# Kernel tuning notes

Hardware: AMD Instinct MI355X
Metric: run time of the kernel (lower is better)

## Reference

```python
import jax, jax.numpy as jnp
import numpy as np

B, S, F, HS = 64, 512, 512, 1024


def _xavier(key, shape):
    fan_in, fan_out = shape
    limit = np.sqrt(6.0 / (fan_in + fan_out))
    return jax.random.uniform(key, shape, jnp.float32, -limit, limit)


def setup_inputs() -> dict:
    key = jax.random.key(0)
    k1, k2, k3 = jax.random.split(key, 3)
    x = jax.random.normal(k1, (B, S, F), jnp.float32)
    weight_ih = _xavier(k2, (F, 3 * HS))
    weight_hh = _xavier(k3, (HS, 3 * HS))
    # bias: zeros except the r-gate slice [HS:2HS] initialized to ones (per init_weights)
    bias = jnp.zeros((3 * HS,), jnp.float32).at[HS:2 * HS].set(1.0)
    return {"x": x, "weight_ih": weight_ih, "weight_hh": weight_hh, "bias": bias}


def reference(x, weight_ih, weight_hh, bias):
    hs = weight_hh.shape[0]
    bsz = x.shape[0]
    # Precompute input-side gates for all timesteps; bias folds in additively
    # (for eta gate: gx_e + r*tanh(gh_e) + b_e  ==  (gx_e + b_e) + r*tanh(gh_e)).
    gx = jnp.einsum('bsf,fg->bsg', x, weight_ih) + bias  # [B,S,3H]

    def step(h, gx_t):
        gh = h @ weight_hh  # [B,3H]
        z = jax.nn.sigmoid(gx_t[:, :hs] + gh[:, :hs])
        r = jax.nn.sigmoid(gx_t[:, hs:2 * hs] + gh[:, hs:2 * hs])
        eta = jnp.tanh(gx_t[:, 2 * hs:] + r * jnp.tanh(gh[:, 2 * hs:]))
        h_new = z * h + (1.0 - z) * eta
        return h_new, h_new

    h0 = jnp.zeros((bsz, hs), x.dtype)
    h_last, hseq = jax.lax.scan(step, h0, jnp.swapaxes(gx, 0, 1))  # hseq: [S,B,H]
    hidden_seq = jnp.swapaxes(hseq, 0, 1)  # [B,S,H]
    return hidden_seq, h_last
```

## Files before the change

kernel.cpp:

```cpp
#include <hip/hip_runtime.h>
#include <math.h>


#define B_   64
#define S_   512
#define F_   512
#define H_   1024
#define KTOT 1536
#define NG   4096
#define NWG  256
#define NTHR 512
#define RS   1544
#define CPS  324
#define SMEM_BYTES (2 * 16 * RS * 2 + 32 * CPS * 4)

typedef short short8 __attribute__((ext_vector_type(8)));
typedef float floatx4 __attribute__((ext_vector_type(4)));

__device__ __forceinline__ float bf2f(unsigned short u) {
    union { unsigned int i; float f; } v; v.i = ((unsigned int)u) << 16; return v.f;
}
__device__ __forceinline__ unsigned short f2bf(float f) {
    union { float f; unsigned int i; } v; v.f = f;
    unsigned int x = v.i;
    x += 0x7fffu + ((x >> 16) & 1u);
    return (unsigned short)(x >> 16);
}
__device__ __forceinline__ void split2(float v, unsigned short& hi, unsigned short& lo) {
    hi = f2bf(v);
    lo = f2bf(v - bf2f(hi));
}
__device__ __forceinline__ float tanh_fast(float a) {
    float e = __expf(-2.f * fabsf(a));
    float t = (1.f - e) / (1.f + e);
    return copysignf(t, a);
}

__global__ void pack_w(const float* __restrict__ Wih,
                       const float* __restrict__ Whh,
                       unsigned short* __restrict__ Whi,
                       unsigned short* __restrict__ Wlo) {
    int idx = blockIdx.x * 256 + threadIdx.x;
    int p = idx / KTOT;
    int k = idx - p * KTOT;
    int j = p >> 2, g = p & 3;
    float v = 0.f;
    if (g == 0)      v = (k < F_) ? Wih[k * 3072 + j]        : Whh[(k - F_) * 3072 + j];
    else if (g == 1) v = (k < F_) ? Wih[k * 3072 + 1024 + j] : Whh[(k - F_) * 3072 + 1024 + j];
    else if (g == 2) { if (k <  F_) v = Wih[k * 3072 + 2048 + j]; }
    else             { if (k >= F_) v = Whh[(k - F_) * 3072 + 2048 + j]; }
    unsigned short hi, lo; split2(v, hi, lo);
    Whi[idx] = hi; Wlo[idx] = lo;
}

__global__ void pack_x(const float* __restrict__ x,
                       unsigned short* __restrict__ xhi,
                       unsigned short* __restrict__ xlo) {
    int idx = blockIdx.x * 256 + threadIdx.x;
    unsigned short hi, lo; split2(x[idx], hi, lo);
    xhi[idx] = hi; xlo[idx] = lo;
}

__device__ __forceinline__ void ks_step_x(floatx4* acc,
    const unsigned short* __restrict__ Ahi, const unsigned short* __restrict__ Alo,
    size_t aofs, const unsigned short* Bh_, const unsigned short* Bl_, int bofs)
{
    short8 bh = *(const short8*)&Bh_[bofs];
    short8 bl = *(const short8*)&Bl_[bofs];
    #pragma unroll
    for (int mt = 0; mt < 4; ++mt) {
        size_t o = aofs + (size_t)mt * ((size_t)16 * S_ * F_);
        short8 ah = *(const short8*)&Ahi[o];
        short8 al = *(const short8*)&Alo[o];
        acc[mt] = __builtin_amdgcn_mfma_f32_16x16x32_bf16(ah, bh, acc[mt], 0, 0, 0);
        acc[mt] = __builtin_amdgcn_mfma_f32_16x16x32_bf16(ah, bl, acc[mt], 0, 0, 0);
        acc[mt] = __builtin_amdgcn_mfma_f32_16x16x32_bf16(al, bh, acc[mt], 0, 0, 0);
    }
}

#define LOADH(A, OFS) \
    asm volatile( \
        "global_load_dwordx4 %0, %[q0], off offset:" OFS " sc0 sc1\n\t" \
        "global_load_dwordx4 %1, %[q1], off offset:" OFS " sc0 sc1\n\t" \
        "global_load_dwordx4 %2, %[q2], off offset:" OFS " sc0 sc1\n\t" \
        "global_load_dwordx4 %3, %[q3], off offset:" OFS " sc0 sc1\n\t" \
        "global_load_dwordx4 %4, %[q4], off offset:" OFS " sc0 sc1\n\t" \
        "global_load_dwordx4 %5, %[q5], off offset:" OFS " sc0 sc1\n\t" \
        "global_load_dwordx4 %6, %[q6], off offset:" OFS " sc0 sc1\n\t" \
        "global_load_dwordx4 %7, %[q7], off offset:" OFS " sc0 sc1" \
        : "=&v"(A[0]), "=&v"(A[1]), "=&v"(A[2]), "=&v"(A[3]), \
          "=&v"(A[4]), "=&v"(A[5]), "=&v"(A[6]), "=&v"(A[7]) \
        : [q0]"v"(ph0), [q1]"v"(pl0), [q2]"v"(ph1), [q3]"v"(pl1), \
          [q4]"v"(ph2), [q5]"v"(pl2), [q6]"v"(ph3), [q7]"v"(pl3) \
        : "memory")

#define WAITVM(N) do { \
        asm volatile("s_waitcnt vmcnt(" #N ")" ::: "memory"); \
        __builtin_amdgcn_sched_barrier(0); \
    } while (0)

#define MFMAS(A, BH, BL) \
    acc[0] = __builtin_amdgcn_mfma_f32_16x16x32_bf16(A[0], BH, acc[0], 0, 0, 0); \
    acc[0] = __builtin_amdgcn_mfma_f32_16x16x32_bf16(A[0], BL, acc[0], 0, 0, 0); \
    acc[0] = __builtin_amdgcn_mfma_f32_16x16x32_bf16(A[1], BH, acc[0], 0, 0, 0); \
    acc[1] = __builtin_amdgcn_mfma_f32_16x16x32_bf16(A[2], BH, acc[1], 0, 0, 0); \
    acc[1] = __builtin_amdgcn_mfma_f32_16x16x32_bf16(A[2], BL, acc[1], 0, 0, 0); \
    acc[1] = __builtin_amdgcn_mfma_f32_16x16x32_bf16(A[3], BH, acc[1], 0, 0, 0); \
    acc[2] = __builtin_amdgcn_mfma_f32_16x16x32_bf16(A[4], BH, acc[2], 0, 0, 0); \
    acc[2] = __builtin_amdgcn_mfma_f32_16x16x32_bf16(A[4], BL, acc[2], 0, 0, 0); \
    acc[2] = __builtin_amdgcn_mfma_f32_16x16x32_bf16(A[5], BH, acc[2], 0, 0, 0); \
    acc[3] = __builtin_amdgcn_mfma_f32_16x16x32_bf16(A[6], BH, acc[3], 0, 0, 0); \
    acc[3] = __builtin_amdgcn_mfma_f32_16x16x32_bf16(A[6], BL, acc[3], 0, 0, 0); \
    acc[3] = __builtin_amdgcn_mfma_f32_16x16x32_bf16(A[7], BH, acc[3], 0, 0, 0)

__global__ __launch_bounds__(NTHR, 2) void gru_persist(
    const unsigned short* __restrict__ xhi,
    const unsigned short* __restrict__ xlo,
    const unsigned short* __restrict__ Whi,
    const unsigned short* __restrict__ Wlo,
    const float* __restrict__ bias,
    float* __restrict__ hf,
    unsigned short* hhi0, unsigned short* hlo0,
    unsigned short* hhi1, unsigned short* hlo1,
    float* __restrict__ out,
    float* __restrict__ hlast,
    unsigned* bar)
{
    extern __shared__ char smem[];
    unsigned short* Bh = (unsigned short*)smem;
    unsigned short* Bl = Bh + 16 * RS;
    float* Cp = (float*)(smem + 2 * 16 * RS * 2);

    const int tid = threadIdx.x;
    const int wg  = blockIdx.x;

    for (int c = tid; c < 16 * 192; c += NTHR) {
        int row = c / 192, c8 = c - row * 192;
        size_t gofs = (size_t)(wg * 16 + row) * KTOT + c8 * 8;
        *(short8*)&Bh[row * RS + c8 * 8] = *(const short8*)&Whi[gofs];
        *(short8*)&Bl[row * RS + c8 * 8] = *(const short8*)&Wlo[gofs];
    }
    __syncthreads();

    const int lane = tid & 63;
    const int kw   = tid >> 6;
    const int l15  = lane & 15, quad = lane >> 4;
    const int xk0   = kw * 64;
    const int hk0   = kw * 128;
    const int bofsx = l15 * RS + xk0 + quad * 8;
    const int bofsh = l15 * RS + 512 + hk0 + quad * 8;

    const int eb   = tid & 63;
    const int ejj  = (tid >> 6) & 3;
    const int ecol = wg * 4 + ejj;
    float bZ = 0.f, bR = 0.f, bE = 0.f;
    if (tid < 256) {
        bZ = bias[ecol];
        bR = bias[H_ + ecol];
        bE = bias[2 * H_ + ecol];
    }
    const int emt = eb >> 4, erow = eb & 15;
    const int err = erow & 3;
    const int cbase = 80 * (erow >> 2) + err;
    const int ehidx = eb * H_ + ecol;

    const size_t hrow = (size_t)l15 * H_ + quad * 8;
    const int cpw = lane * 4 + (lane >> 2) * 4;

    floatx4 z4v = {0.f, 0.f, 0.f, 0.f};

    floatx4 accx[4] = {z4v, z4v, z4v, z4v};
    {
        const size_t xrow0 = ((size_t)l15 * S_) * F_ + quad * 8;
        #pragma unroll
        for (int ks = 0; ks < 2; ++ks)
            ks_step_x(accx, xhi, xlo, xrow0 + xk0 + ks * 32, Bh, Bl, bofsx + ks * 32);
    }

    for (int t = 0; t < S_; ++t) {
        const unsigned short* hih = (t & 1) ? hhi1 : hhi0;
        const unsigned short* hil = (t & 1) ? hlo1 : hlo0;
        unsigned short* hoh = (t & 1) ? hhi0 : hhi1;
        unsigned short* hol = (t & 1) ? hlo0 : hlo1;

        floatx4 acc[4] = {accx[0], accx[1], accx[2], accx[3]};

        short8 bhv[4], blv[4];
        #pragma unroll
        for (int ks = 0; ks < 4; ++ks) {
            bhv[ks] = *(const short8*)&Bh[bofsh + ks * 32];
            blv[ks] = *(const short8*)&Bl[bofsh + ks * 32];
        }

        const unsigned short* ph0 = hih + hrow + hk0;
        const unsigned short* pl0 = hil + hrow + hk0;
        const unsigned short* ph1 = ph0 + 16 * H_;
        const unsigned short* pl1 = pl0 + 16 * H_;
        const unsigned short* ph2 = ph0 + 32 * H_;
        const unsigned short* pl2 = pl0 + 32 * H_;
        const unsigned short* ph3 = ph0 + 48 * H_;
        const unsigned short* pl3 = pl0 + 48 * H_;

        short8 hv0[8], hv1[8], hv2[8], hv3[8];
        LOADH(hv0, "0");
        LOADH(hv1, "64");
        LOADH(hv2, "128");
        LOADH(hv3, "192");

        WAITVM(24); MFMAS(hv0, bhv[0], blv[0]);
        WAITVM(16); MFMAS(hv1, bhv[1], blv[1]);
        WAITVM(8);  MFMAS(hv2, bhv[2], blv[2]);
        WAITVM(0);  MFMAS(hv3, bhv[3], blv[3]);

        #pragma unroll
        for (int mt = 0; mt < 4; ++mt)
            *(floatx4*)&Cp[(kw * 4 + mt) * CPS + cpw] = acc[mt];
        __syncthreads();

        float hn = 0.f;
        if (tid < 256) {
            float g[4];
            #pragma unroll
            for (int gi = 0; gi < 4; ++gi) {
                const int c = ejj * 4 + gi;
                const int coff = cbase + 4 * c + 4 * (c >> 2);
                float s = 0.f;
                #pragma unroll
                for (int k2 = 0; k2 < 8; ++k2)
                    s += Cp[(k2 * 4 + emt) * CPS + coff];
                g[gi] = s;
            }
            float z   = 1.f / (1.f + __expf(-(g[0] + bZ)));
            float rr  = 1.f / (1.f + __expf(-(g[1] + bR)));
            float eta = tanh_fast(g[2] + bE + rr * tanh_fast(g[3]));
            float ho  = hf[ehidx];
            hn = z * ho + (1.f - z) * eta;
            unsigned short hi, lo; split2(hn, hi, lo);
            asm volatile("global_store_short %0, %1, off sc0 sc1"
                         :: "v"(&hoh[ehidx]), "v"((unsigned)hi) : "memory");
            asm volatile("global_store_short %0, %1, off sc0 sc1"
                         :: "v"(&hol[ehidx]), "v"((unsigned)lo) : "memory");
        }
        asm volatile("s_waitcnt vmcnt(0)" ::: "memory");
        __syncthreads();
        if (tid == 0)
            __hip_atomic_fetch_add(&bar[(wg & 7) * 32], 1u,
                                   __ATOMIC_RELAXED, __HIP_MEMORY_SCOPE_AGENT);

        if (tid < 256) {
            hf[ehidx] = hn;
            out[((size_t)eb * S_ + t) * H_ + ecol] = hn;
            if (t == S_ - 1) hlast[ehidx] = hn;
        }

        if (t + 1 < S_) {
            #pragma unroll
            for (int mt = 0; mt < 4; ++mt) accx[mt] = z4v;
            const size_t xrow = ((size_t)l15 * S_ + (t + 1)) * F_ + quad * 8;
            #pragma unroll
            for (int ks = 0; ks < 2; ++ks)
                ks_step_x(accx, xhi, xlo, xrow + xk0 + ks * 32, Bh, Bl, bofsx + ks * 32);
        }

        if (tid == 0) {
            const unsigned target = (unsigned)(t + 1) * NWG;
            for (;;) {
                unsigned c0, c1, c2, c3, c4, c5, c6, c7;
                asm volatile(
                    "global_load_dword %0, %[a0], off sc0 sc1\n\t"
                    "global_load_dword %1, %[a1], off sc0 sc1\n\t"
                    "global_load_dword %2, %[a2], off sc0 sc1\n\t"
                    "global_load_dword %3, %[a3], off sc0 sc1\n\t"
                    "global_load_dword %4, %[a4], off sc0 sc1\n\t"
                    "global_load_dword %5, %[a5], off sc0 sc1\n\t"
                    "global_load_dword %6, %[a6], off sc0 sc1\n\t"
                    "global_load_dword %7, %[a7], off sc0 sc1\n\t"
                    "s_waitcnt vmcnt(0)"
                    : "=&v"(c0), "=&v"(c1), "=&v"(c2), "=&v"(c3),
                      "=&v"(c4), "=&v"(c5), "=&v"(c6), "=&v"(c7)
                    : [a0]"v"(bar),       [a1]"v"(bar + 32),
                      [a2]"v"(bar + 64),  [a3]"v"(bar + 96),
                      [a4]"v"(bar + 128), [a5]"v"(bar + 160),
                      [a6]"v"(bar + 192), [a7]"v"(bar + 224)
                    : "memory");
                if (c0 + c1 + c2 + c3 + c4 + c5 + c6 + c7 >= target) break;
                __builtin_amdgcn_s_sleep(1);
            }
        }
        __syncthreads();
    }
}

extern "C" void kernel_launch(void* const* d_in, const int* in_sizes, int n_in,
                              void* d_out, int out_size, void* d_ws, size_t ws_size,
                              hipStream_t stream) {
    const float* x    = (const float*)d_in[0];
    const float* Wih  = (const float*)d_in[1];
    const float* Whh  = (const float*)d_in[2];
    const float* bias = (const float*)d_in[3];
    float* out = (float*)d_out;

    char* ws = (char*)d_ws;
    unsigned short* Whi = (unsigned short*)ws; ws += (size_t)NG * KTOT * 2;
    unsigned short* Wlo = (unsigned short*)ws; ws += (size_t)NG * KTOT * 2;
    unsigned short* xhi = (unsigned short*)ws; ws += (size_t)B_ * S_ * F_ * 2;
    unsigned short* xlo = (unsigned short*)ws; ws += (size_t)B_ * S_ * F_ * 2;
    float* hf = (float*)ws;                    ws += (size_t)B_ * H_ * 4;
    unsigned short* hhi0 = (unsigned short*)ws; ws += (size_t)B_ * H_ * 2;
    unsigned short* hlo0 = (unsigned short*)ws; ws += (size_t)B_ * H_ * 2;
    unsigned short* hhi1 = (unsigned short*)ws; ws += (size_t)B_ * H_ * 2;
    unsigned short* hlo1 = (unsigned short*)ws; ws += (size_t)B_ * H_ * 2;
    unsigned* bar = (unsigned*)ws;             ws += 1024;

    hipMemsetAsync(hf,   0, (size_t)B_ * H_ * 4, stream);
    hipMemsetAsync(hhi0, 0, (size_t)B_ * H_ * 2, stream);
    hipMemsetAsync(hlo0, 0, (size_t)B_ * H_ * 2, stream);
    hipMemsetAsync(bar,  0, 1024, stream);

    pack_w<<<(NG * KTOT) / 256, 256, 0, stream>>>(Wih, Whh, Whi, Wlo);
    pack_x<<<(B_ * S_ * F_) / 256, 256, 0, stream>>>(x, xhi, xlo);

    float* hlast = out + (size_t)B_ * S_ * H_;
    void* args[] = { &xhi, &xlo, &Whi, &Wlo, &bias, &hf,
                     &hhi0, &hlo0, &hhi1, &hlo1, &out, &hlast, &bar };
    hipLaunchCooperativeKernel((void*)gru_persist, dim3(NWG), dim3(NTHR),
                               args, SMEM_BYTES, stream);
}
```

Measured before the change: 7.455 ms.

## Keep hidden state in registers and vectorize per-step epilogue stores

The per-step epilogue moves from 256 threads handling one column each to 64 threads each handling four adjacent columns. The fp32 hidden state now stays in registers instead of being reloaded from a global buffer every step, and the hi/lo and output stores become dwordx2/dwordx4 vector stores issued before the barrier. The hand-scheduled inline-asm h loads with staged waitcnts are replaced by compiler-generated loads behind an acquire fence. This trades fewer global round trips and store instructions for less epilogue parallelism and possibly worse load/MFMA overlap.

```diff
diff --git a/kernel.cpp b/kernel.cpp
--- a/kernel.cpp
+++ b/kernel.cpp
@@ -16,6 +16,7 @@
 
 typedef short short8 __attribute__((ext_vector_type(8)));
 typedef float floatx4 __attribute__((ext_vector_type(4)));
+typedef unsigned int uint2v __attribute__((ext_vector_type(2)));
 
 __device__ __forceinline__ float bf2f(unsigned short u) {
     union { unsigned int i; float f; } v; v.i = ((unsigned int)u) << 16; return v.f;
@@ -78,40 +79,22 @@
     }
 }
 
-#define LOADH(A, OFS) \
-    asm volatile( \
-        "global_load_dwordx4 %0, %[q0], off offset:" OFS " sc0 sc1\n\t" \
-        "global_load_dwordx4 %1, %[q1], off offset:" OFS " sc0 sc1\n\t" \
-        "global_load_dwordx4 %2, %[q2], off offset:" OFS " sc0 sc1\n\t" \
-        "global_load_dwordx4 %3, %[q3], off offset:" OFS " sc0 sc1\n\t" \
-        "global_load_dwordx4 %4, %[q4], off offset:" OFS " sc0 sc1\n\t" \
-        "global_load_dwordx4 %5, %[q5], off offset:" OFS " sc0 sc1\n\t" \
-        "global_load_dwordx4 %6, %[q6], off offset:" OFS " sc0 sc1\n\t" \
-        "global_load_dwordx4 %7, %[q7], off offset:" OFS " sc0 sc1" \
-        : "=&v"(A[0]), "=&v"(A[1]), "=&v"(A[2]), "=&v"(A[3]), \
-          "=&v"(A[4]), "=&v"(A[5]), "=&v"(A[6]), "=&v"(A[7]) \
-        : [q0]"v"(ph0), [q1]"v"(pl0), [q2]"v"(ph1), [q3]"v"(pl1), \
-          [q4]"v"(ph2), [q5]"v"(pl2), [q6]"v"(ph3), [q7]"v"(pl3) \
-        : "memory")
-
-#define WAITVM(N) do { \
-        asm volatile("s_waitcnt vmcnt(" #N ")" ::: "memory"); \
-        __builtin_amdgcn_sched_barrier(0); \
-    } while (0)
-
-#define MFMAS(A, BH, BL) \
-    acc[0] = __builtin_amdgcn_mfma_f32_16x16x32_bf16(A[0], BH, acc[0], 0, 0, 0); \
-    acc[0] = __builtin_amdgcn_mfma_f32_16x16x32_bf16(A[0], BL, acc[0], 0, 0, 0); \
-    acc[0] = __builtin_amdgcn_mfma_f32_16x16x32_bf16(A[1], BH, acc[0], 0, 0, 0); \
-    acc[1] = __builtin_amdgcn_mfma_f32_16x16x32_bf16(A[2], BH, acc[1], 0, 0, 0); \
-    acc[1] = __builtin_amdgcn_mfma_f32_16x16x32_bf16(A[2], BL, acc[1], 0, 0, 0); \
-    acc[1] = __builtin_amdgcn_mfma_f32_16x16x32_bf16(A[3], BH, acc[1], 0, 0, 0); \
-    acc[2] = __builtin_amdgcn_mfma_f32_16x16x32_bf16(A[4], BH, acc[2], 0, 0, 0); \
-    acc[2] = __builtin_amdgcn_mfma_f32_16x16x32_bf16(A[4], BL, acc[2], 0, 0, 0); \
-    acc[2] = __builtin_amdgcn_mfma_f32_16x16x32_bf16(A[5], BH, acc[2], 0, 0, 0); \
-    acc[3] = __builtin_amdgcn_mfma_f32_16x16x32_bf16(A[6], BH, acc[3], 0, 0, 0); \
-    acc[3] = __builtin_amdgcn_mfma_f32_16x16x32_bf16(A[6], BL, acc[3], 0, 0, 0); \
-    acc[3] = __builtin_amdgcn_mfma_f32_16x16x32_bf16(A[7], BH, acc[3], 0, 0, 0)
+__device__ __forceinline__ void ks_step_h_c(floatx4* acc,
+    const unsigned short* Hhi, const unsigned short* Hlo, size_t aofs,
+    const unsigned short* Bh_, const unsigned short* Bl_, int bofs)
+{
+    short8 bh = *(const short8*)&Bh_[bofs];
+    short8 bl = *(const short8*)&Bl_[bofs];
+    #pragma unroll
+    for (int mt = 0; mt < 4; ++mt) {
+        size_t o = aofs + (size_t)mt * ((size_t)16 * H_);
+        short8 ah = *(const short8*)&Hhi[o];
+        short8 al = *(const short8*)&Hlo[o];
+        acc[mt] = __builtin_amdgcn_mfma_f32_16x16x32_bf16(ah, bh, acc[mt], 0, 0, 0);
+        acc[mt] = __builtin_amdgcn_mfma_f32_16x16x32_bf16(ah, bl, acc[mt], 0, 0, 0);
+        acc[mt] = __builtin_amdgcn_mfma_f32_16x16x32_bf16(al, bh, acc[mt], 0, 0, 0);
+    }
+}
 
 __global__ __launch_bounds__(NTHR, 2) void gru_persist(
     const unsigned short* __restrict__ xhi,
@@ -119,7 +102,6 @@
     const unsigned short* __restrict__ Whi,
     const unsigned short* __restrict__ Wlo,
     const float* __restrict__ bias,
-    float* __restrict__ hf,
     unsigned short* hhi0, unsigned short* hlo0,
     unsigned short* hhi1, unsigned short* hlo1,
     float* __restrict__ out,
@@ -150,22 +132,20 @@
     const int bofsx = l15 * RS + xk0 + quad * 8;
     const int bofsh = l15 * RS + 512 + hk0 + quad * 8;
 
-    const int eb   = tid & 63;
-    const int ejj  = (tid >> 6) & 3;
-    const int ecol = wg * 4 + ejj;
-    float bZ = 0.f, bR = 0.f, bE = 0.f;
-    if (tid < 256) {
-        bZ = bias[ecol];
-        bR = bias[H_ + ecol];
-        bE = bias[2 * H_ + ecol];
-    }
-    const int emt = eb >> 4, erow = eb & 15;
-    const int err = erow & 3;
-    const int cbase = 80 * (erow >> 2) + err;
-    const int ehidx = eb * H_ + ecol;
+    floatx4 bZ4 = {0,0,0,0}, bR4 = {0,0,0,0}, bE4 = {0,0,0,0};
+    if (tid < 64) {
+        bZ4 = *(const floatx4*)&bias[wg * 4];
+        bR4 = *(const floatx4*)&bias[H_ + wg * 4];
+        bE4 = *(const floatx4*)&bias[2 * H_ + wg * 4];
+    }
+    const int emt  = (tid >> 4) & 3, erow = tid & 15;
+    const int cbase = 80 * (erow >> 2) + (erow & 3);
+    const int hbidx = tid * H_ + wg * 4;
 
     const size_t hrow = (size_t)l15 * H_ + quad * 8;
     const int cpw = lane * 4 + (lane >> 2) * 4;
+
+    float hcur[4] = {0.f, 0.f, 0.f, 0.f};
 
     floatx4 z4v = {0.f, 0.f, 0.f, 0.f};
 
@@ -183,75 +163,60 @@
         unsigned short* hoh = (t & 1) ? hhi0 : hhi1;
         unsigned short* hol = (t & 1) ? hlo0 : hlo1;
 
+        __builtin_amdgcn_fence(__ATOMIC_ACQUIRE, "agent");
+
         floatx4 acc[4] = {accx[0], accx[1], accx[2], accx[3]};
-
-        short8 bhv[4], blv[4];
         #pragma unroll
-        for (int ks = 0; ks < 4; ++ks) {
-            bhv[ks] = *(const short8*)&Bh[bofsh + ks * 32];
-            blv[ks] = *(const short8*)&Bl[bofsh + ks * 32];
-        }
-
-        const unsigned short* ph0 = hih + hrow + hk0;
-        const unsigned short* pl0 = hil + hrow + hk0;
-        const unsigned short* ph1 = ph0 + 16 * H_;
-        const unsigned short* pl1 = pl0 + 16 * H_;
-        const unsigned short* ph2 = ph0 + 32 * H_;
-        const unsigned short* pl2 = pl0 + 32 * H_;
-        const unsigned short* ph3 = ph0 + 48 * H_;
-        const unsigned short* pl3 = pl0 + 48 * H_;
-
-        short8 hv0[8], hv1[8], hv2[8], hv3[8];
-        LOADH(hv0, "0");
-        LOADH(hv1, "64");
-        LOADH(hv2, "128");
-        LOADH(hv3, "192");
-
-        WAITVM(24); MFMAS(hv0, bhv[0], blv[0]);
-        WAITVM(16); MFMAS(hv1, bhv[1], blv[1]);
-        WAITVM(8);  MFMAS(hv2, bhv[2], blv[2]);
-        WAITVM(0);  MFMAS(hv3, bhv[3], blv[3]);
+        for (int ks = 0; ks < 4; ++ks)
+            ks_step_h_c(acc, hih, hil, hrow + hk0 + ks * 32, Bh, Bl, bofsh + ks * 32);
 
         #pragma unroll
         for (int mt = 0; mt < 4; ++mt)
             *(floatx4*)&Cp[(kw * 4 + mt) * CPS + cpw] = acc[mt];
         __syncthreads();
 
-        float hn = 0.f;
-        if (tid < 256) {
-            float g[4];
+        if (tid < 64) {
+            float hn[4]; unsigned short his[4], los[4];
             #pragma unroll
-            for (int gi = 0; gi < 4; ++gi) {
-                const int c = ejj * 4 + gi;
-                const int coff = cbase + 4 * c + 4 * (c >> 2);
-                float s = 0.f;
+            for (int j = 0; j < 4; ++j) {
+                float s[4];
                 #pragma unroll
-                for (int k2 = 0; k2 < 8; ++k2)
-                    s += Cp[(k2 * 4 + emt) * CPS + coff];
-                g[gi] = s;
+                for (int gi = 0; gi < 4; ++gi) {
+                    const int coff = cbase + 20 * j + 4 * gi;
+                    float a = 0.f;
+                    #pragma unroll
+                    for (int k2 = 0; k2 < 8; ++k2)
+                        a += Cp[(k2 * 4 + emt) * CPS + coff];
+                    s[gi] = a;
+                }
+                float z   = 1.f / (1.f + __expf(-(s[0] + bZ4[j])));
+                float rr  = 1.f / (1.f + __expf(-(s[1] + bR4[j])));
+                float eta = tanh_fast(s[2] + bE4[j] + rr * tanh_fast(s[3]));
+                float v   = z * hcur[j] + (1.f - z) * eta;
+                hcur[j] = v; hn[j] = v;
+                split2(v, his[j], los[j]);
             }
-            float z   = 1.f / (1.f + __expf(-(g[0] + bZ)));
-            float rr  = 1.f / (1.f + __expf(-(g[1] + bR)));
-            float eta = tanh_fast(g[2] + bE + rr * tanh_fast(g[3]));
-            float ho  = hf[ehidx];
-            hn = z * ho + (1.f - z) * eta;
-            unsigned short hi, lo; split2(hn, hi, lo);
-            asm volatile("global_store_short %0, %1, off sc0 sc1"
-                         :: "v"(&hoh[ehidx]), "v"((unsigned)hi) : "memory");
-            asm volatile("global_store_short %0, %1, off sc0 sc1"
-                         :: "v"(&hol[ehidx]), "v"((unsigned)lo) : "memory");
+            uint2v hp = { (unsigned)his[0] | ((unsigned)his[1] << 16),
+                          (unsigned)his[2] | ((unsigned)his[3] << 16) };
+            uint2v lp = { (unsigned)los[0] | ((unsigned)los[1] << 16),
+                          (unsigned)los[2] | ((unsigned)los[3] << 16) };
+            floatx4 ov = { hn[0], hn[1], hn[2], hn[3] };
+            asm volatile("global_store_dwordx2 %0, %1, off sc0 sc1"
+                         :: "v"(&hoh[hbidx]), "v"(hp) : "memory");
+            asm volatile("global_store_dwordx2 %0, %1, off sc0 sc1"
+                         :: "v"(&hol[hbidx]), "v"(lp) : "memory");
+            asm volatile("global_store_dwordx4 %0, %1, off sc0 sc1"
+                         :: "v"(&out[((size_t)tid * S_ + t) * H_ + wg * 4]), "v"(ov)
+                         : "memory");
+            if (t == S_ - 1)
+                asm volatile("global_store_dwordx4 %0, %1, off sc0 sc1"
+                             :: "v"(&hlast[hbidx]), "v"(ov) : "memory");
         }
         asm volatile("s_waitcnt vmcnt(0)" ::: "memory");
         __syncthreads();
         if (tid == 0)
             __hip_atomic_fetch_add(&bar[(wg & 7) * 32], 1u,
                                    __ATOMIC_RELAXED, __HIP_MEMORY_SCOPE_AGENT);
-
-        if (tid < 256) {
-            hf[ehidx] = hn;
-            out[((size_t)eb * S_ + t) * H_ + ecol] = hn;
-            if (t == S_ - 1) hlast[ehidx] = hn;
-        }
 
         if (t + 1 < S_) {
             #pragma unroll
@@ -305,14 +270,12 @@
     unsigned short* Wlo = (unsigned short*)ws; ws += (size_t)NG * KTOT * 2;
     unsigned short* xhi = (unsigned short*)ws; ws += (size_t)B_ * S_ * F_ * 2;
     unsigned short* xlo = (unsigned short*)ws; ws += (size_t)B_ * S_ * F_ * 2;
-    float* hf = (float*)ws;                    ws += (size_t)B_ * H_ * 4;
     unsigned short* hhi0 = (unsigned short*)ws; ws += (size_t)B_ * H_ * 2;
     unsigned short* hlo0 = (unsigned short*)ws; ws += (size_t)B_ * H_ * 2;
     unsigned short* hhi1 = (unsigned short*)ws; ws += (size_t)B_ * H_ * 2;
     unsigned short* hlo1 = (unsigned short*)ws; ws += (size_t)B_ * H_ * 2;
     unsigned* bar = (unsigned*)ws;             ws += 1024;
 
-    hipMemsetAsync(hf,   0, (size_t)B_ * H_ * 4, stream);
     hipMemsetAsync(hhi0, 0, (size_t)B_ * H_ * 2, stream);
     hipMemsetAsync(hlo0, 0, (size_t)B_ * H_ * 2, stream);
     hipMemsetAsync(bar,  0, 1024, stream);
@@ -321,7 +284,7 @@
     pack_x<<<(B_ * S_ * F_) / 256, 256, 0, stream>>>(x, xhi, xlo);
 
     float* hlast = out + (size_t)B_ * S_ * H_;
-    void* args[] = { &xhi, &xlo, &Whi, &Wlo, &bias, &hf,
+    void* args[] = { &xhi, &xlo, &Whi, &Wlo, &bias,
                      &hhi0, &hlo0, &hhi1, &hlo1, &out, &hlast, &bar };
     hipLaunchCooperativeKernel((void*)gru_persist, dim3(NWG), dim3(NTHR),
                                args, SMEM_BYTES, stream);
```

After: 13.91 ms. 1.87x slower.
